# Kernel tuning notes

Hardware: AMD Instinct MI355X
Metric: run time of the kernel (lower is better)

Reference implementation:

```python
import jax, jax.numpy as jnp
import numpy as np

H = 16          # num_heads
EPS = 1e-5      # torch LayerNorm default eps


def setup_inputs() -> dict:
    key = jax.random.key(0)
    ks = jax.random.split(key, 12)
    B, S, D = 4, 2048, 1024
    sc = 1.0 / np.sqrt(D)
    return {
        "queries": jax.random.normal(ks[0], (B, S, D), jnp.float32),
        "keys": jax.random.normal(ks[1], (B, S, D), jnp.float32),
        "values": jax.random.normal(ks[2], (B, S, D), jnp.float32),
        "attention_mask": jax.random.randint(ks[3], (B, S), 0, 2, jnp.int32),
        "Wq": jax.random.normal(ks[4], (D, D), jnp.float32) * sc,
        "bq": jnp.zeros((D,), jnp.float32),
        "Wk": jax.random.normal(ks[5], (D, D), jnp.float32) * sc,
        "bk": jnp.zeros((D,), jnp.float32),
        "Wv": jax.random.normal(ks[6], (D, D), jnp.float32) * sc,
        "bv": jnp.zeros((D,), jnp.float32),
        "gamma": jnp.ones((D,), jnp.float32),
        "beta": jnp.zeros((D,), jnp.float32),
    }


def reference(queries, keys, values, attention_mask, Wq, bq, Wk, bk, Wv, bv, gamma, beta):
    B, S, D = queries.shape
    dh = D // H

    # QKV projections with ReLU epilogue (nn.Sequential(Linear, ReLU))
    q = jax.nn.relu(jnp.einsum("bsd,de->bse", queries, Wq) + bq)
    k = jax.nn.relu(jnp.einsum("bsd,de->bse", keys, Wk) + bk)
    v = jax.nn.relu(jnp.einsum("bsd,de->bse", values, Wv) + bv)

    # chunk along last dim + stack at dim=1  ==  [B,S,H,dh] -> [B,H,S,dh]
    q_ = q.reshape(B, S, H, dh).transpose(0, 2, 1, 3)
    k_ = k.reshape(B, S, H, dh).transpose(0, 2, 1, 3)
    v_ = v.reshape(B, S, H, dh).transpose(0, 2, 1, 3)

    # scaled dot-product scores [B,H,S,S]
    scores = jnp.einsum("bhqd,bhkd->bhqk", q_, k_) / jnp.sqrt(jnp.float32(dh))

    # mask[b,h,i,j] = attention_mask[b,i]; masked positions set to 1e-9
    # (faithful to torch.masked_fill(value=1e-09) in the original)
    m = attention_mask[:, None, :, None].astype(bool)  # [B,1,S,1]
    scores = jnp.where(m, scores, jnp.float32(1e-9))

    a = jax.nn.softmax(scores, axis=-1)
    o = jnp.einsum("bhqk,bhkd->bhqd", a, v_)          # [B,H,S,dh]
    o = o.transpose(0, 2, 1, 3).reshape(B, S, D)

    # residual + LayerNorm
    x = o + queries
    mu = jnp.mean(x, axis=-1, keepdims=True)
    var = jnp.mean(jnp.square(x - mu), axis=-1, keepdims=True)
    return (x - mu) * jax.lax.rsqrt(var + EPS) * gamma + beta
```

## Files before the change

kernel.cpp:

```cpp
#include <hip/hip_runtime.h>
#include <hip/hip_bf16.h>
#include <stdint.h>

typedef __bf16 bf16x8 __attribute__((ext_vector_type(8)));
typedef float f32x4 __attribute__((ext_vector_type(4)));
typedef float f32x16 __attribute__((ext_vector_type(16)));
typedef unsigned short ushort8v __attribute__((ext_vector_type(8)));
typedef unsigned short ushort4v __attribute__((ext_vector_type(4)));
typedef uint32_t uint4v __attribute__((ext_vector_type(4)));

#define MFMA16(a, b, c) __builtin_amdgcn_mfma_f32_16x16x32_bf16(a, b, c, 0, 0, 0)
#define MFMA32(a, b, c) __builtin_amdgcn_mfma_f32_32x32x16_bf16(a, b, c, 0, 0, 0)

#define GLOAD_LDS16(g, l)                                                        \
    __builtin_amdgcn_global_load_lds(                                            \
        (const __attribute__((address_space(1))) uint32_t*)(g),                  \
        (__attribute__((address_space(3))) uint32_t*)(l), 16, 0, 0)

#define QSCALE 0.1803368801f

__device__ __forceinline__ unsigned short f2bf_u(float f) {
    union { float f; uint32_t u; } cv; cv.f = f;
    uint32_t u = cv.u;
    uint32_t r = (u + 0x7FFFu + ((u >> 16) & 1u)) >> 16;
    return (unsigned short)r;
}

__device__ __forceinline__ float bf2f(unsigned short u) {
    union { uint32_t u; float f; } cv;
    cv.u = (uint32_t)u << 16;
    return cv.f;
}

__device__ __forceinline__ uint32_t pkbf(float a, float b) {
    union { __hip_bfloat162 h; uint32_t u; } cv;
    cv.h = __float22bfloat162_rn(make_float2(a, b));
    return cv.u;
}

__device__ __forceinline__ float fexp2(float x) { return __builtin_amdgcn_exp2f(x); }

__global__ __launch_bounds__(256) void wt_cast(const float* __restrict__ W0,
                                               const float* __restrict__ W1,
                                               const float* __restrict__ W2,
                                               unsigned short* __restrict__ T0,
                                               unsigned short* __restrict__ T1,
                                               unsigned short* __restrict__ T2) {
    const int z = blockIdx.z;
    const float* W = z == 0 ? W0 : (z == 1 ? W1 : W2);
    unsigned short* Wt = z == 0 ? T0 : (z == 1 ? T1 : T2);
    __shared__ float t[32][33];
    const int tx = threadIdx.x & 31, ty = threadIdx.x >> 5;
    const int n0 = blockIdx.x * 32, k0 = blockIdx.y * 32;
#pragma unroll
    for (int i = 0; i < 4; i++) {
        int r = i * 8 + ty;
        t[r][tx] = W[(size_t)(k0 + r) * 1024 + n0 + tx];
    }
    __syncthreads();
#pragma unroll
    for (int i = 0; i < 4; i++) {
        int r = i * 8 + ty;
        Wt[(size_t)(n0 + r) * 1024 + k0 + tx] = f2bf_u(t[tx][r]);
    }
}

__global__ __launch_bounds__(256) void acast(const float* __restrict__ A0,
                                             const float* __restrict__ A1,
                                             const float* __restrict__ A2,
                                             unsigned short* __restrict__ B0,
                                             unsigned short* __restrict__ B1,
                                             unsigned short* __restrict__ B2) {
    const int z = blockIdx.y;
    const float* A = z == 0 ? A0 : (z == 1 ? A1 : A2);
    unsigned short* B = z == 0 ? B0 : (z == 1 ? B1 : B2);
    const size_t i = ((size_t)blockIdx.x * 256 + threadIdx.x) * 8;
    const float4 f0 = *reinterpret_cast<const float4*>(A + i);
    const float4 f1 = *reinterpret_cast<const float4*>(A + i + 4);
    uint4v u;
    u[0] = pkbf(f0.x, f0.y);
    u[1] = pkbf(f0.z, f0.w);
    u[2] = pkbf(f1.x, f1.y);
    u[3] = pkbf(f1.z, f1.w);
    *reinterpret_cast<uint4v*>(B + i) = u;
}

__global__ __launch_bounds__(256) void qkv_gemm3(
    const unsigned short* __restrict__ Aq, const unsigned short* __restrict__ Ak,
    const unsigned short* __restrict__ Av,
    const unsigned short* __restrict__ Wq, const unsigned short* __restrict__ Wk,
    const unsigned short* __restrict__ Wv,
    const float* __restrict__ biasq, const float* __restrict__ biask,
    const float* __restrict__ biasv, const int* __restrict__ mask,
    unsigned short* __restrict__ outq, unsigned short* __restrict__ outk,
    unsigned short* __restrict__ outv) {
    __shared__ __align__(16) unsigned short aS[2][128 * 32];
    __shared__ __align__(16) unsigned short wS[2][128 * 32];
    const int id = blockIdx.x;
    const int xcd = id & 7;
    const int local = id >> 3;
    const int z = local >> 6;
    const int l2i = local & 63;
    const int m0 = (xcd * 8 + (l2i >> 3)) * 128;
    const int n0 = (l2i & 7) * 128;

    const unsigned short* A = z == 0 ? Aq : (z == 1 ? Ak : Av);
    const unsigned short* Wt = z == 0 ? Wq : (z == 1 ? Wk : Wv);
    const float* bias = z == 0 ? biasq : (z == 1 ? biask : biasv);
    unsigned short* out = z == 0 ? outq : (z == 1 ? outk : outv);
    const bool vt = (z == 2);

    const int tid = threadIdx.x;
    const int lane = tid & 63, wave = tid >> 6;
    const int rrow = lane & 15, rgrp = lane >> 4;
    const int wm = wave >> 1, wn = wave & 1;

    const int row0 = tid >> 2, c0 = tid & 3;
    const int row1 = (tid + 256) >> 2;
    const int arow_f = wm * 64 + rrow;
    const int brow_f = wn * 64 + rrow;

    f32x4 acc[4][4];
#pragma unroll
    for (int i = 0; i < 4; i++)
#pragma unroll
        for (int j = 0; j < 4; j++) acc[i][j] = (f32x4)0.0f;

    auto STAGE = [&](const unsigned short* src, int r0, int k0, void* dstbase) {
        char* dst = (char*)dstbase + wave * 1024;
        GLOAD_LDS16((const char*)src + ((size_t)(r0 + row0) * 1024 + k0 + c0 * 8) * 2, dst);
        GLOAD_LDS16((const char*)src + ((size_t)(r0 + row1) * 1024 + k0 + c0 * 8) * 2,
                    dst + 4096);
    };

    STAGE(A, m0, 0, &aS[0][0]);
    STAGE(Wt, n0, 0, &wS[0][0]);
    __syncthreads();

    for (int ks = 0; ks < 32; ks++) {
        const int cur = ks & 1;
        if (ks < 31) {
            STAGE(A, m0, (ks + 1) * 32, &aS[cur ^ 1][0]);
            STAGE(Wt, n0, (ks + 1) * 32, &wS[cur ^ 1][0]);
        }

        bf16x8 af[4], bfr[4];
#pragma unroll
        for (int mi = 0; mi < 4; mi++)
            af[mi] = *reinterpret_cast<const bf16x8*>(
                (const char*)&aS[cur][0] + (arow_f + mi * 16) * 64 + rgrp * 16);
#pragma unroll
        for (int ni = 0; ni < 4; ni++)
            bfr[ni] = *reinterpret_cast<const bf16x8*>(
                (const char*)&wS[cur][0] + (brow_f + ni * 16) * 64 + rgrp * 16);
        __builtin_amdgcn_s_setprio(1);
#pragma unroll
        for (int mi = 0; mi < 4; mi++)
#pragma unroll
            for (int ni = 0; ni < 4; ni++)
                acc[mi][ni] = MFMA16(af[mi], bfr[ni], acc[mi][ni]);
        __builtin_amdgcn_s_setprio(0);

        __syncthreads();
    }

#pragma unroll
    for (int mi = 0; mi < 4; mi++) {
        const int mbase = m0 + wm * 64 + mi * 16 + rgrp * 4;
        const int b = mbase >> 11, s = mbase & 2047;
        float qs[4];
#pragma unroll
        for (int jr = 0; jr < 4; jr++)
            qs[jr] = (z != 0) ? 1.0f : (mask[b * 2048 + s + jr] ? QSCALE : 0.0f);
#pragma unroll
        for (int ni = 0; ni < 4; ni++) {
            const int n = n0 + wn * 64 + ni * 16 + rrow;
            const float bv = bias[n];
            const int h = n >> 6, d = n & 63;
            if (vt) {
                ushort4v pv;
#pragma unroll
                for (int jr = 0; jr < 4; jr++)
                    pv[jr] = f2bf_u(fmaxf(acc[mi][ni][jr] + bv, 0.0f));
                *reinterpret_cast<ushort4v*>(out + ((size_t)((b * 16 + h) * 64 + d)) * 2048 + s) = pv;
            } else {
#pragma unroll
                for (int jr = 0; jr < 4; jr++)
                    out[((size_t)((b * 16 + h) * 2048 + (s + jr))) * 64 + d] =
                        f2bf_u(fmaxf(acc[mi][ni][jr] + bv, 0.0f) * qs[jr]);
            }
        }
    }
}

__global__ __launch_bounds__(256, 4) void flash_attn(const unsigned short* __restrict__ Qg,
                                                     const unsigned short* __restrict__ Kg,
                                                     const unsigned short* __restrict__ Vt,
                                                     unsigned short* __restrict__ O) {
    __shared__ __align__(16) unsigned short ldsK[2][64 * 64];
    __shared__ __align__(16) unsigned short ldsV[2][64 * 64];
    const int tid = threadIdx.x;
    const int lane = tid & 63, wave = tid >> 6;
    const int c = lane & 31, hi = lane >> 5;
    const int bid = blockIdx.x;
    const int swzb = (bid & 7) * 128 + (bid >> 3);
    const int gid = swzb * 4 + wave;
    const int bh = gid >> 6;
    const int q0 = (gid & 63) * 32;
    const int b = bh >> 4, h = bh & 15;
    const size_t base = (size_t)bh * (2048 * 64);
    const unsigned short* Qb = Qg + base;
    const unsigned short* Kb = Kg + base;
    const unsigned short* Vb = Vt + base;

    const int srow = lane >> 3;
    const int schunk = (lane & 7) ^ srow;
    int offL[4], offH[4];
#pragma unroll
    for (int ds = 0; ds < 4; ds++) {
        offL[ds] = c * 128 + ((((ds << 1) + hi) ^ (c & 7)) << 4);
        offH[ds] = offL[ds] + 32 * 128;
    }

    bf16x8 qf[4];
#pragma unroll
    for (int ds = 0; ds < 4; ds++)
        qf[ds] = *reinterpret_cast<const bf16x8*>(Qb + (size_t)(q0 + c) * 64 + ds * 16 + hi * 8);

    union { uint32_t u[4]; bf16x8 v; } onesf;
#pragma unroll
    for (int i = 0; i < 4; i++) onesf.u[i] = 0x3F803F80u;

    f32x16 lacc = (f32x16)0.0f;
    f32x16 oacc0 = (f32x16)0.0f, oacc1 = (f32x16)0.0f;

    auto STAGE = [&](int kt, int bufi) {
        const char* ktile = (const char*)Kb + (size_t)kt * 8192;
        const char* vtile = (const char*)Vb + (size_t)kt * 128;
        char* kdst = (char*)&ldsK[bufi][0] + wave * 2048;
        char* vdst = (char*)&ldsV[bufi][0] + wave * 2048;
#pragma unroll
        for (int i = 0; i < 2; i++) {
            const int row = wave * 16 + i * 8 + srow;
            GLOAD_LDS16(ktile + row * 128 + schunk * 16, kdst + i * 1024);
            GLOAD_LDS16(vtile + (size_t)row * 4096 + schunk * 16, vdst + i * 1024);
        }
    };

    STAGE(0, 0);
    __syncthreads();

    for (int kt = 0; kt < 32; kt++) {
        const int cur = kt & 1;
        if (kt < 31) STAGE(kt + 1, cur ^ 1);
        const char* kbuf = (const char*)&ldsK[cur][0];
        const char* vbuf = (const char*)&ldsV[cur][0];

        f32x16 sacc0 = (f32x16)0.0f, sacc1 = (f32x16)0.0f;
        __builtin_amdgcn_s_setprio(1);
#pragma unroll
        for (int ds = 0; ds < 4; ds++) {
            bf16x8 k0 = *reinterpret_cast<const bf16x8*>(kbuf + offL[ds]);
            bf16x8 k1 = *reinterpret_cast<const bf16x8*>(kbuf + offH[ds]);
            sacc0 = MFMA32(k0, qf[ds], sacc0);
            sacc1 = MFMA32(k1, qf[ds], sacc1);
        }
        __builtin_amdgcn_s_setprio(0);

#pragma unroll
        for (int j = 0; j < 16; j++) {
            sacc0[j] = fexp2(sacc0[j]);
            sacc1[j] = fexp2(sacc1[j]);
        }

        {
            uint32_t w0[8];
#pragma unroll
            for (int i = 0; i < 8; i++) w0[i] = pkbf(sacc0[2 * i], sacc0[2 * i + 1]);
            asm("v_permlane32_swap_b32 %0, %1" : "+v"(w0[0]), "+v"(w0[2]));
            asm("v_permlane32_swap_b32 %0, %1" : "+v"(w0[1]), "+v"(w0[3]));
            asm("v_permlane32_swap_b32 %0, %1" : "+v"(w0[4]), "+v"(w0[6]));
            asm("v_permlane32_swap_b32 %0, %1" : "+v"(w0[5]), "+v"(w0[7]));
            union { uint32_t u[4]; bf16x8 v; } pa[2];
            pa[0].u[0] = w0[0]; pa[0].u[1] = w0[1]; pa[0].u[2] = w0[2]; pa[0].u[3] = w0[3];
            pa[1].u[0] = w0[4]; pa[1].u[1] = w0[5]; pa[1].u[2] = w0[6]; pa[1].u[3] = w0[7];
            __builtin_amdgcn_s_setprio(1);
#pragma unroll
            for (int ks = 0; ks < 2; ks++) {
                bf16x8 v0 = *reinterpret_cast<const bf16x8*>(vbuf + offL[ks]);
                bf16x8 v1 = *reinterpret_cast<const bf16x8*>(vbuf + offH[ks]);
                lacc = MFMA32(pa[ks].v, onesf.v, lacc);
                oacc0 = MFMA32(pa[ks].v, v0, oacc0);
                oacc1 = MFMA32(pa[ks].v, v1, oacc1);
            }
            __builtin_amdgcn_s_setprio(0);
        }
        {
            uint32_t w1[8];
#pragma unroll
            for (int i = 0; i < 8; i++) w1[i] = pkbf(sacc1[2 * i], sacc1[2 * i + 1]);
            asm("v_permlane32_swap_b32 %0, %1" : "+v"(w1[0]), "+v"(w1[2]));
            asm("v_permlane32_swap_b32 %0, %1" : "+v"(w1[1]), "+v"(w1[3]));
            asm("v_permlane32_swap_b32 %0, %1" : "+v"(w1[4]), "+v"(w1[6]));
            asm("v_permlane32_swap_b32 %0, %1" : "+v"(w1[5]), "+v"(w1[7]));
            union { uint32_t u[4]; bf16x8 v; } pa[2];
            pa[0].u[0] = w1[0]; pa[0].u[1] = w1[1]; pa[0].u[2] = w1[2]; pa[0].u[3] = w1[3];
            pa[1].u[0] = w1[4]; pa[1].u[1] = w1[5]; pa[1].u[2] = w1[6]; pa[1].u[3] = w1[7];
            __builtin_amdgcn_s_setprio(1);
#pragma unroll
            for (int ks = 0; ks < 2; ks++) {
                bf16x8 v0 = *reinterpret_cast<const bf16x8*>(vbuf + offL[2 + ks]);
                bf16x8 v1 = *reinterpret_cast<const bf16x8*>(vbuf + offH[2 + ks]);
                lacc = MFMA32(pa[ks].v, onesf.v, lacc);
                oacc0 = MFMA32(pa[ks].v, v0, oacc0);
                oacc1 = MFMA32(pa[ks].v, v1, oacc1);
            }
            __builtin_amdgcn_s_setprio(0);
        }

        __syncthreads();
    }

#pragma unroll
    for (int reg = 0; reg < 16; reg++) {
        const int rr = (reg & 3) + 8 * (reg >> 2) + 4 * hi;
        const float ir = 1.0f / lacc[reg];
        const size_t rowoff = (size_t)(b * 2048 + q0 + rr) * 1024 + h * 64 + c;
        O[rowoff]      = f2bf_u(oacc0[reg] * ir);
        O[rowoff + 32] = f2bf_u(oacc1[reg] * ir);
    }
}

__global__ __launch_bounds__(256) void resid_ln(const unsigned short* __restrict__ O,
                                                const unsigned short* __restrict__ Qin,
                                                const float* __restrict__ gamma,
                                                const float* __restrict__ beta,
                                                float* __restrict__ out) {
    __shared__ float red[4];
    const int row = blockIdx.x, tid = threadIdx.x;
    const size_t base = (size_t)row * 1024 + tid * 4;
    const ushort4v o4 = *reinterpret_cast<const ushort4v*>(O + base);
    const ushort4v q4 = *reinterpret_cast<const ushort4v*>(Qin + base);
    float x0 = bf2f(o4[0]) + bf2f(q4[0]), x1 = bf2f(o4[1]) + bf2f(q4[1]);
    float x2 = bf2f(o4[2]) + bf2f(q4[2]), x3 = bf2f(o4[3]) + bf2f(q4[3]);

    float s = x0 + x1 + x2 + x3;
#pragma unroll
    for (int off = 32; off >= 1; off >>= 1) s += __shfl_xor(s, off, 64);
    const int w = tid >> 6;
    if ((tid & 63) == 0) red[w] = s;
    __syncthreads();
    const float mean = (red[0] + red[1] + red[2] + red[3]) * (1.0f / 1024.0f);
    __syncthreads();

    const float d0 = x0 - mean, d1 = x1 - mean, d2 = x2 - mean, d3 = x3 - mean;
    float vs = d0 * d0 + d1 * d1 + d2 * d2 + d3 * d3;
#pragma unroll
    for (int off = 32; off >= 1; off >>= 1) vs += __shfl_xor(vs, off, 64);
    if ((tid & 63) == 0) red[w] = vs;
    __syncthreads();
    const float var = (red[0] + red[1] + red[2] + red[3]) * (1.0f / 1024.0f);
    const float rstd = rsqrtf(var + 1e-5f);

    float4 g = *reinterpret_cast<const float4*>(gamma + tid * 4);
    float4 be = *reinterpret_cast<const float4*>(beta + tid * 4);
    float4 r;
    r.x = d0 * rstd * g.x + be.x;
    r.y = d1 * rstd * g.y + be.y;
    r.z = d2 * rstd * g.z + be.z;
    r.w = d3 * rstd * g.w + be.w;
    *reinterpret_cast<float4*>(out + base) = r;
}

extern "C" void kernel_launch(void* const* d_in, const int* in_sizes, int n_in,
                              void* d_out, int out_size, void* d_ws, size_t ws_size,
                              hipStream_t stream) {
    const float* q_in = (const float*)d_in[0];
    const float* k_in = (const float*)d_in[1];
    const float* v_in = (const float*)d_in[2];
    const int* mask = (const int*)d_in[3];
    const float* Wq = (const float*)d_in[4];
    const float* bq = (const float*)d_in[5];
    const float* Wk = (const float*)d_in[6];
    const float* bk = (const float*)d_in[7];
    const float* Wv = (const float*)d_in[8];
    const float* bv = (const float*)d_in[9];
    const float* gamma = (const float*)d_in[10];
    const float* beta = (const float*)d_in[11];
    float* out = (float*)d_out;

    unsigned short* wtq = (unsigned short*)d_ws;
    unsigned short* wtk = wtq + 1024 * 1024;
    unsigned short* wtv = wtk + 1024 * 1024;
    unsigned short* Qb = wtv + 1024 * 1024;
    unsigned short* Kb = Qb + 8192 * 1024;
    unsigned short* Vtb = Kb + 8192 * 1024;
    unsigned short* Aqb = Vtb + 8192 * 1024;
    unsigned short* Akb = Aqb + 8192 * 1024;
    unsigned short* Avb = Akb + 8192 * 1024;
    unsigned short* Obuf = Avb;

    dim3 tb(256);
    wt_cast<<<dim3(32, 32, 3), tb, 0, stream>>>(Wq, Wk, Wv, wtq, wtk, wtv);
    acast<<<dim3(4096, 3), tb, 0, stream>>>(q_in, k_in, v_in, Aqb, Akb, Avb);
    qkv_gemm3<<<dim3(1536), tb, 0, stream>>>(Aqb, Akb, Avb, wtq, wtk, wtv,
                                             bq, bk, bv, mask, Qb, Kb, Vtb);
    flash_attn<<<dim3(1024), tb, 0, stream>>>(Qb, Kb, Vtb, Obuf);
    resid_ln<<<dim3(8192), tb, 0, stream>>>(Obuf, Aqb, gamma, beta, out);
}
```

Baseline: 190.7 us.

## Fuse fp32-to-bf16 activation cast into QKV GEMM A-tile loading

Removes the separate acast kernel and has the QKV GEMM load fp32 activations through registers, convert them to bf16 and write them into LDS, with the load issued one step ahead for software pipelining. The residual LayerNorm now reads the original fp32 queries instead of a bf16 copy. This avoids writing and re-reading three bf16 activation buffers plus one launch. In exchange the GEMM reads twice as many bytes for A, uses extra registers and ordinary vector loads instead of direct global-to-LDS loads.

```diff
diff --git a/kernel.cpp b/kernel.cpp
--- a/kernel.cpp
+++ b/kernel.cpp
@@ -7,6 +7,7 @@
 typedef float f32x16 __attribute__((ext_vector_type(16)));
 typedef unsigned short ushort8v __attribute__((ext_vector_type(8)));
 typedef unsigned short ushort4v __attribute__((ext_vector_type(4)));
+typedef uint32_t uint2v __attribute__((ext_vector_type(2)));
 typedef uint32_t uint4v __attribute__((ext_vector_type(4)));
 
 #define MFMA16(a, b, c) __builtin_amdgcn_mfma_f32_16x16x32_bf16(a, b, c, 0, 0, 0)
@@ -65,29 +66,9 @@
     }
 }
 
-__global__ __launch_bounds__(256) void acast(const float* __restrict__ A0,
-                                             const float* __restrict__ A1,
-                                             const float* __restrict__ A2,
-                                             unsigned short* __restrict__ B0,
-                                             unsigned short* __restrict__ B1,
-                                             unsigned short* __restrict__ B2) {
-    const int z = blockIdx.y;
-    const float* A = z == 0 ? A0 : (z == 1 ? A1 : A2);
-    unsigned short* B = z == 0 ? B0 : (z == 1 ? B1 : B2);
-    const size_t i = ((size_t)blockIdx.x * 256 + threadIdx.x) * 8;
-    const float4 f0 = *reinterpret_cast<const float4*>(A + i);
-    const float4 f1 = *reinterpret_cast<const float4*>(A + i + 4);
-    uint4v u;
-    u[0] = pkbf(f0.x, f0.y);
-    u[1] = pkbf(f0.z, f0.w);
-    u[2] = pkbf(f1.x, f1.y);
-    u[3] = pkbf(f1.z, f1.w);
-    *reinterpret_cast<uint4v*>(B + i) = u;
-}
-
-__global__ __launch_bounds__(256) void qkv_gemm3(
-    const unsigned short* __restrict__ Aq, const unsigned short* __restrict__ Ak,
-    const unsigned short* __restrict__ Av,
+__global__ __launch_bounds__(256) void qkv_gemm4(
+    const float* __restrict__ Aq, const float* __restrict__ Ak,
+    const float* __restrict__ Av,
     const unsigned short* __restrict__ Wq, const unsigned short* __restrict__ Wk,
     const unsigned short* __restrict__ Wv,
     const float* __restrict__ biasq, const float* __restrict__ biask,
@@ -104,7 +85,7 @@
     const int m0 = (xcd * 8 + (l2i >> 3)) * 128;
     const int n0 = (l2i & 7) * 128;
 
-    const unsigned short* A = z == 0 ? Aq : (z == 1 ? Ak : Av);
+    const float* A = z == 0 ? Aq : (z == 1 ? Ak : Av);
     const unsigned short* Wt = z == 0 ? Wq : (z == 1 ? Wk : Wv);
     const float* bias = z == 0 ? biasq : (z == 1 ? biask : biasv);
     unsigned short* out = z == 0 ? outq : (z == 1 ? outk : outv);
@@ -126,22 +107,43 @@
 #pragma unroll
         for (int j = 0; j < 4; j++) acc[i][j] = (f32x4)0.0f;
 
-    auto STAGE = [&](const unsigned short* src, int r0, int k0, void* dstbase) {
-        char* dst = (char*)dstbase + wave * 1024;
-        GLOAD_LDS16((const char*)src + ((size_t)(r0 + row0) * 1024 + k0 + c0 * 8) * 2, dst);
-        GLOAD_LDS16((const char*)src + ((size_t)(r0 + row1) * 1024 + k0 + c0 * 8) * 2,
+    auto STAGE_W = [&](int k0, int bufi) {
+        char* dst = (char*)&wS[bufi][0] + wave * 1024;
+        GLOAD_LDS16((const char*)Wt + ((size_t)(n0 + row0) * 1024 + k0 + c0 * 8) * 2, dst);
+        GLOAD_LDS16((const char*)Wt + ((size_t)(n0 + row1) * 1024 + k0 + c0 * 8) * 2,
                     dst + 4096);
     };
-
-    STAGE(A, m0, 0, &aS[0][0]);
-    STAGE(Wt, n0, 0, &wS[0][0]);
+    auto LOAD_A = [&](int k0, float4* r) {
+#pragma unroll
+        for (int i = 0; i < 4; i++) {
+            const int g = i * 256 + tid, row = g >> 3, qc = g & 7;
+            r[i] = *reinterpret_cast<const float4*>(A + (size_t)(m0 + row) * 1024 + k0 + qc * 4);
+        }
+    };
+    auto WRITE_A = [&](const float4* r, int bufi) {
+#pragma unroll
+        for (int i = 0; i < 4; i++) {
+            const int g = i * 256 + tid, row = g >> 3, qc = g & 7;
+            uint2v w;
+            w[0] = pkbf(r[i].x, r[i].y);
+            w[1] = pkbf(r[i].z, r[i].w);
+            *reinterpret_cast<uint2v*>((char*)&aS[bufi][0] + row * 64 + qc * 8) = w;
+        }
+    };
+
+    float4 aload[4];
+    LOAD_A(0, aload);
+    STAGE_W(0, 0);
+    WRITE_A(aload, 0);
+    LOAD_A(32, aload);
     __syncthreads();
 
     for (int ks = 0; ks < 32; ks++) {
         const int cur = ks & 1;
         if (ks < 31) {
-            STAGE(A, m0, (ks + 1) * 32, &aS[cur ^ 1][0]);
-            STAGE(Wt, n0, (ks + 1) * 32, &wS[cur ^ 1][0]);
+            WRITE_A(aload, cur ^ 1);
+            STAGE_W((ks + 1) * 32, cur ^ 1);
+            if (ks < 30) LOAD_A((ks + 2) * 32, aload);
         }
 
         bf16x8 af[4], bfr[4];
@@ -332,7 +334,7 @@
 }
 
 __global__ __launch_bounds__(256) void resid_ln(const unsigned short* __restrict__ O,
-                                                const unsigned short* __restrict__ Qin,
+                                                const float* __restrict__ Qin,
                                                 const float* __restrict__ gamma,
                                                 const float* __restrict__ beta,
                                                 float* __restrict__ out) {
@@ -340,9 +342,9 @@
     const int row = blockIdx.x, tid = threadIdx.x;
     const size_t base = (size_t)row * 1024 + tid * 4;
     const ushort4v o4 = *reinterpret_cast<const ushort4v*>(O + base);
-    const ushort4v q4 = *reinterpret_cast<const ushort4v*>(Qin + base);
-    float x0 = bf2f(o4[0]) + bf2f(q4[0]), x1 = bf2f(o4[1]) + bf2f(q4[1]);
-    float x2 = bf2f(o4[2]) + bf2f(q4[2]), x3 = bf2f(o4[3]) + bf2f(q4[3]);
+    const float4 q4 = *reinterpret_cast<const float4*>(Qin + base);
+    float x0 = bf2f(o4[0]) + q4.x, x1 = bf2f(o4[1]) + q4.y;
+    float x2 = bf2f(o4[2]) + q4.z, x3 = bf2f(o4[3]) + q4.w;
 
     float s = x0 + x1 + x2 + x3;
 #pragma unroll
@@ -395,16 +397,12 @@
     unsigned short* Qb = wtv + 1024 * 1024;
     unsigned short* Kb = Qb + 8192 * 1024;
     unsigned short* Vtb = Kb + 8192 * 1024;
-    unsigned short* Aqb = Vtb + 8192 * 1024;
-    unsigned short* Akb = Aqb + 8192 * 1024;
-    unsigned short* Avb = Akb + 8192 * 1024;
-    unsigned short* Obuf = Avb;
+    unsigned short* Obuf = Vtb + 8192 * 1024;
 
     dim3 tb(256);
     wt_cast<<<dim3(32, 32, 3), tb, 0, stream>>>(Wq, Wk, Wv, wtq, wtk, wtv);
-    acast<<<dim3(4096, 3), tb, 0, stream>>>(q_in, k_in, v_in, Aqb, Akb, Avb);
-    qkv_gemm3<<<dim3(1536), tb, 0, stream>>>(Aqb, Akb, Avb, wtq, wtk, wtv,
+    qkv_gemm4<<<dim3(1536), tb, 0, stream>>>(q_in, k_in, v_in, wtq, wtk, wtv,
                                              bq, bk, bv, mask, Qb, Kb, Vtb);
     flash_attn<<<dim3(1024), tb, 0, stream>>>(Qb, Kb, Vtb, Obuf);
-    resid_ln<<<dim3(8192), tb, 0, stream>>>(Obuf, Aqb, gamma, beta, out);
-}
+    resid_ln<<<dim3(8192), tb, 0, stream>>>(Obuf, q_in, gamma, beta, out);
+}
```

After: 179.1 us, median of 2. 6.1% less time.
